# Kernel tuning notes

Hardware: AMD Instinct MI355X
Metric: run time of the kernel (lower is better)

## Reference

```python
import jax, jax.numpy as jnp
import numpy as np

EMBED_DIM = 1024
NUM_HEADS = 16
HEAD_DIM = EMBED_DIM // NUM_HEADS
EPSILON = 1e-6
SCORE_SCALE = 1.0
B, L = 2, 2048


def setup_inputs() -> dict:
    key = jax.random.key(0)
    k0, k1, k2, k3, k4 = jax.random.split(key, 5)
    s_in = 1.0 / np.sqrt(EMBED_DIM)
    return {
        "x": jax.random.normal(k0, (B, L, EMBED_DIM), dtype=jnp.float32),
        "w_qkv": jax.random.normal(k1, (EMBED_DIM, 3 * EMBED_DIM), dtype=jnp.float32) * s_in,
        "b_qkv": jnp.zeros((3 * EMBED_DIM,), dtype=jnp.float32),
        "w_out": jax.random.normal(k2, (EMBED_DIM, EMBED_DIM), dtype=jnp.float32) * s_in,
        "b_out": jnp.zeros((EMBED_DIM,), dtype=jnp.float32),
    }


def reference(x, w_qkv, b_qkv, w_out, b_out):
    Bq, Lq, E = x.shape
    qkv = x @ w_qkv + b_qkv  # [B, L, 3E]
    q, k, v = jnp.split(qkv, 3, axis=-1)
    q = q.reshape(Bq, Lq, NUM_HEADS, HEAD_DIM).transpose(0, 2, 1, 3)  # bhld
    k = k.reshape(Bq, Lq, NUM_HEADS, HEAD_DIM).transpose(0, 2, 1, 3)
    v = v.reshape(Bq, Lq, NUM_HEADS, HEAD_DIM).transpose(0, 2, 1, 3)

    dot = jnp.einsum('bhid,bhjd->bhij', q, k)
    q_norm_sq = jnp.sum(q * q, axis=-1, keepdims=True)          # [b,h,L,1]
    k_norm_sq = jnp.sum(k * k, axis=-1, keepdims=True)          # [b,h,L,1]
    vals = q_norm_sq + k_norm_sq.transpose(0, 1, 3, 2)          # [b,h,L,L]
    scores = (dot * dot) / (vals - 2.0 * dot + EPSILON) * SCORE_SCALE

    mask = jnp.triu(jnp.ones((Lq, Lq), dtype=scores.dtype), k=1) * -1e9
    scores = scores + mask[None, None, :, :]
    attn = jax.nn.softmax(scores, axis=-1)
    out = jnp.einsum('bhij,bhjd->bhid', attn, v)
    out = out.transpose(0, 2, 1, 3).reshape(Bq, Lq, E)
    return out @ w_out + b_out
```

## Files before the change

kernel.cpp:

```cpp
#include <hip/hip_runtime.h>

#define EMBED 1024
#define NH 16
#define HD 64
#define SEQ 2048
#define BATCH 2
#define ROWS (BATCH*SEQ)
#define BHD (BATCH*NH)

typedef __bf16 bf16x8 __attribute__((ext_vector_type(8)));
typedef _Float16 f16x4 __attribute__((ext_vector_type(4)));
typedef float f32x4 __attribute__((ext_vector_type(4)));

__device__ __forceinline__ unsigned short f2bf(float f){
  union { float f; unsigned u; } v; v.f = f;
  unsigned r = v.u + 0x7fffu + ((v.u >> 16) & 1u);
  return (unsigned short)(r >> 16);
}
__device__ __forceinline__ float bf2f(unsigned short s){
  union { unsigned u; float f; } v; v.u = ((unsigned)s) << 16; return v.f;
}
__device__ __forceinline__ unsigned short f2h(float f){
  union { _Float16 h; unsigned short u; } v; v.h = (_Float16)f; return v.u;
}

typedef __attribute__((address_space(1))) unsigned int as1_t;
typedef __attribute__((address_space(3))) unsigned int as3_t;
__device__ __forceinline__ void async_ld16(const void* gp, void* lp){
  __builtin_amdgcn_global_load_lds((as1_t*)gp, (as3_t*)lp, 16, 0, 0);
}


__global__ __launch_bounds__(256) void k_conv(const float* __restrict__ x,
                                              unsigned short* __restrict__ xb, int n4){
  int i = blockIdx.x * blockDim.x + threadIdx.x;
  if (i < n4){
    float4 f = ((const float4*)x)[i];
    ushort4 o;
    o.x = f2bf(f.x); o.y = f2bf(f.y); o.z = f2bf(f.z); o.w = f2bf(f.w);
    ((ushort4*)xb)[i] = o;
  }
}

__global__ __launch_bounds__(256) void k_tr_f2b(const float* __restrict__ in,
                                                unsigned short* __restrict__ out, int R, int C){
  __shared__ float t[32][33];
  int c0 = blockIdx.x * 32, r0 = blockIdx.y * 32;
  int tx = threadIdx.x, ty = threadIdx.y;
  #pragma unroll
  for (int i = 0; i < 4; i++){ int r = ty + i*8; t[r][tx] = in[(size_t)(r0+r)*C + c0 + tx]; }
  __syncthreads();
  #pragma unroll
  for (int i = 0; i < 4; i++){ int rr = ty + i*8; out[(size_t)(c0+rr)*R + r0 + tx] = f2bf(t[tx][rr]); }
}

__global__ __launch_bounds__(256) void k_tr_b2b(const unsigned short* __restrict__ in,
                                                unsigned short* __restrict__ out, int R, int C){
  in  += (size_t)blockIdx.z * R * C;
  out += (size_t)blockIdx.z * R * C;
  __shared__ unsigned short t[32][33];
  int c0 = blockIdx.x * 32, r0 = blockIdx.y * 32;
  int tx = threadIdx.x, ty = threadIdx.y;
  #pragma unroll
  for (int i = 0; i < 4; i++){ int r = ty + i*8; t[r][tx] = in[(size_t)(r0+r)*C + c0 + tx]; }
  __syncthreads();
  #pragma unroll
  for (int i = 0; i < 4; i++){ int rr = ty + i*8; out[(size_t)(c0+rr)*R + r0 + tx] = t[tx][rr]; }
}

__global__ __launch_bounds__(256) void k_norms(const unsigned short* __restrict__ q,
                                               const unsigned short* __restrict__ k,
                                               float* __restrict__ qn, float* __restrict__ kn){
  int i = blockIdx.x * blockDim.x + threadIdx.x;
  const uint4* qr = (const uint4*)(q + (size_t)i * HD);
  const uint4* kr = (const uint4*)(k + (size_t)i * HD);
  float sq = 0.f, sk = 0.f;
  #pragma unroll
  for (int t = 0; t < 8; t++){
    uint4 uq = qr[t], uk = kr[t];
    unsigned aq[4] = {uq.x, uq.y, uq.z, uq.w};
    unsigned ak[4] = {uk.x, uk.y, uk.z, uk.w};
    #pragma unroll
    for (int j = 0; j < 4; j++){
      float f0 = bf2f((unsigned short)(aq[j] & 0xffff));
      float f1 = bf2f((unsigned short)(aq[j] >> 16));
      sq += f0*f0 + f1*f1;
      float g0 = bf2f((unsigned short)(ak[j] & 0xffff));
      float g1 = bf2f((unsigned short)(ak[j] >> 16));
      sk += g0*g0 + g1*g1;
    }
  }
  qn[i] = sq; kn[i] = sk;
}


__global__ __launch_bounds__(256) void k_gemm_qkv(
    const unsigned short* __restrict__ A,
    const unsigned short* __restrict__ BT,
    const float* __restrict__ bias,
    unsigned short* __restrict__ qo, unsigned short* __restrict__ ko,
    unsigned short* __restrict__ vo)
{
  __shared__ __align__(16) unsigned short As[128*32];
  __shared__ __align__(16) unsigned short Bs[128*32];
  const int K = EMBED;
  int m0 = blockIdx.x * 128, n0 = blockIdx.y * 128;
  int tid = threadIdx.x, lane = tid & 63, wave = tid >> 6;
  int wm = wave >> 1, wn = wave & 1;
  int l16 = lane & 15, quad = lane >> 4;
  f32x4 acc[4][4] = {};
  int c0i = wave*64 + lane, c1i = 256 + wave*64 + lane;
  int r0 = c0i >> 2, cc0 = (c0i & 3) * 8;
  int r1 = c1i >> 2, cc1 = (c1i & 3) * 8;
  unsigned short* lA0 = &As[(wave*64)*8];
  unsigned short* lA1 = &As[(256 + wave*64)*8];
  unsigned short* lB0 = &Bs[(wave*64)*8];
  unsigned short* lB1 = &Bs[(256 + wave*64)*8];
  for (int k0 = 0; k0 < K; k0 += 32){
    async_ld16((void*)&A [(size_t)(m0 + r0)*K + k0 + cc0], (void*)lA0);
    async_ld16((void*)&A [(size_t)(m0 + r1)*K + k0 + cc1], (void*)lA1);
    async_ld16((void*)&BT[(size_t)(n0 + r0)*K + k0 + cc0], (void*)lB0);
    async_ld16((void*)&BT[(size_t)(n0 + r1)*K + k0 + cc1], (void*)lB1);
    __syncthreads();
    bf16x8 af[4], bfr[4];
    #pragma unroll
    for (int mi = 0; mi < 4; mi++) af[mi]  = *(const bf16x8*)&As[(wm*64 + mi*16 + l16)*32 + quad*8];
    #pragma unroll
    for (int ni = 0; ni < 4; ni++) bfr[ni] = *(const bf16x8*)&Bs[(wn*64 + ni*16 + l16)*32 + quad*8];
    #pragma unroll
    for (int mi = 0; mi < 4; mi++)
      #pragma unroll
      for (int ni = 0; ni < 4; ni++)
        acc[mi][ni] = __builtin_amdgcn_mfma_f32_16x16x32_bf16(af[mi], bfr[ni], acc[mi][ni], 0, 0, 0);
    __syncthreads();
  }
  #pragma unroll
  for (int mi = 0; mi < 4; mi++)
    #pragma unroll
    for (int ni = 0; ni < 4; ni++)
      #pragma unroll
      for (int rr = 0; rr < 4; rr++){
        int row = m0 + wm*64 + mi*16 + quad*4 + rr;
        int col = n0 + wn*64 + ni*16 + l16;
        float val = acc[mi][ni][rr] + bias[col];
        int b = row >> 11, l = row & 2047;
        int which = col >> 10, e = col & 1023, h = e >> 6, d = e & 63;
        unsigned short* dst = which == 0 ? qo : (which == 1 ? ko : vo);
        unsigned short bits = (which == 2) ? f2h(val) : f2bf(val);
        dst[(((size_t)(b*NH + h))*SEQ + l)*HD + d] = bits;
      }
}


__global__ __launch_bounds__(256) void k_attn(
    const unsigned short* __restrict__ qg,
    const unsigned short* __restrict__ kg,
    const unsigned short* __restrict__ vtg,
    const float* __restrict__ qn,
    const float* __restrict__ kn,
    unsigned short* __restrict__ attn_out)
{
  __shared__ __align__(16) unsigned short Ks[2][2048];
  __shared__ __align__(16) _Float16      Vs[2][2048];
  int bh = blockIdx.y; int b = bh >> 4, h = bh & 15;
  int tid = threadIdx.x, lane = tid & 63, wave = tid >> 6;
  int l16 = lane & 15, quad = lane >> 4;
  int tb = 31 - blockIdx.x;
  int qb = tb * 64;
  int q0 = qb + wave*16;
  int jmax_w = q0 + 16;
  int jmax_b = qb + 64;

  const unsigned short* qbase = qg  + (size_t)bh * SEQ * HD;
  const unsigned short* kbase = kg  + (size_t)bh * SEQ * HD;
  const _Float16*       vtb   = (const _Float16*)vtg + (size_t)bh * HD * SEQ;
  const float* knb = kn + (size_t)bh * SEQ;

  int sI = wave*64 + lane;
  int kj   = sI >> 3;
  int ko16 = (sI & 7) ^ (kj & 7);
  int vd   = sI >> 2;
  int vc2  = (sI & 3) ^ (vd & 3);

  bf16x8 aq[2];
  #pragma unroll
  for (int sk = 0; sk < 2; sk++)
    aq[sk] = *(const bf16x8*)&qbase[(size_t)(q0 + l16)*HD + sk*32 + quad*8];
  float qn_m = qn[(size_t)bh*SEQ + q0 + l16];

  float m_run = -1e30f, l_lane = 0.f;
  f32x4 oacc[4] = {};

  async_ld16((const void*)&kbase[(size_t)kj*HD + ko16*8], (void*)&Ks[0][wave*512]);
  async_ld16((const void*)&vtb[(size_t)vd*SEQ + vc2*8],   (void*)&Vs[0][wave*512]);

  for (int j0 = 0; j0 < jmax_b; j0 += 32){
    int buf = (j0 >> 5) & 1;
    __syncthreads();
    if (j0 + 32 < jmax_b){
      async_ld16((const void*)&kbase[(size_t)(j0 + 32 + kj)*HD + ko16*8], (void*)&Ks[buf^1][wave*512]);
      async_ld16((const void*)&vtb[(size_t)vd*SEQ + (j0 + 32) + vc2*8],   (void*)&Vs[buf^1][wave*512]);
    }
    if (j0 < jmax_w){
      f32x4 st[2] = {};
      #pragma unroll
      for (int tile = 0; tile < 2; tile++)
        #pragma unroll
        for (int sk = 0; sk < 2; sk++){
          bf16x8 ak = *(const bf16x8*)&Ks[buf][((tile*16 + l16)*8 + ((sk*4 + quad) ^ (l16 & 7)))*8];
          st[tile] = __builtin_amdgcn_mfma_f32_16x16x32_bf16(ak, aq[sk], st[tile], 0, 0, 0);
        }
      float4 kn_a = *(const float4*)&knb[j0 + quad*4];
      float4 kn_b = *(const float4*)&knb[j0 + 16 + quad*4];
      float kn_j[2][4] = {{kn_a.x, kn_a.y, kn_a.z, kn_a.w}, {kn_b.x, kn_b.y, kn_b.z, kn_b.w}};
      int mg = q0 + l16;
      float sc[2][4];
      if (j0 + 32 > q0){
        #pragma unroll
        for (int tile = 0; tile < 2; tile++)
          #pragma unroll
          for (int rr = 0; rr < 4; rr++){
            int jg = j0 + tile*16 + quad*4 + rr;
            float dot = st[tile][rr];
            float den = fmaxf(qn_m + kn_j[tile][rr] - 2.0f*dot, 0.0f) + 1e-6f;
            float v = dot * dot * __builtin_amdgcn_rcpf(den);
            sc[tile][rr] = (jg <= mg) ? v : -1e30f;
          }
      } else {
        #pragma unroll
        for (int tile = 0; tile < 2; tile++)
          #pragma unroll
          for (int rr = 0; rr < 4; rr++){
            float dot = st[tile][rr];
            float den = fmaxf(qn_m + kn_j[tile][rr] - 2.0f*dot, 0.0f) + 1e-6f;
            sc[tile][rr] = dot * dot * __builtin_amdgcn_rcpf(den);
          }
      }
      float mx = fmaxf(fmaxf(fmaxf(sc[0][0], sc[0][1]), fmaxf(sc[0][2], sc[0][3])),
                       fmaxf(fmaxf(sc[1][0], sc[1][1]), fmaxf(sc[1][2], sc[1][3])));
      mx = fmaxf(mx, __shfl_xor(mx, 16));
      mx = fmaxf(mx, __shfl_xor(mx, 32));
      float mnew = fmaxf(m_run, mx);
      float alpha = __expf(m_run - mnew);
      m_run = mnew;

      float ps = 0.f;
      #pragma unroll
      for (int tile = 0; tile < 2; tile++)
        #pragma unroll
        for (int rr = 0; rr < 4; rr++){
          float e = __expf(sc[tile][rr] - mnew);
          sc[tile][rr] = e; ps += e;
        }
      l_lane = l_lane * alpha + ps;

      #pragma unroll
      for (int g = 0; g < 4; g++)
        #pragma unroll
        for (int rr = 0; rr < 4; rr++) oacc[g][rr] *= alpha;

      #pragma unroll
      for (int tile = 0; tile < 2; tile++){
        f16x4 pf;
        #pragma unroll
        for (int rr = 0; rr < 4; rr++) pf[rr] = (_Float16)sc[tile][rr];
        #pragma unroll
        for (int g = 0; g < 4; g++){
          f16x4 av = *(const f16x4*)&Vs[buf][(g*16 + l16)*32 + (((tile*2 + (quad>>1)) ^ (l16 & 3))*8) + (quad & 1)*4];
          oacc[g] = __builtin_amdgcn_mfma_f32_16x16x16f16(av, pf, oacc[g], 0, 0, 0);
        }
      }
    }
  }

  float l_tot = l_lane + __shfl_xor(l_lane, 16);
  l_tot += __shfl_xor(l_tot, 32);
  float linv = __builtin_amdgcn_rcpf(l_tot);

  size_t orow = (size_t)(b*SEQ + q0 + l16)*EMBED + h*HD;
  #pragma unroll
  for (int g = 0; g < 4; g++){
    ushort4 pk;
    pk.x = f2bf(oacc[g][0] * linv);
    pk.y = f2bf(oacc[g][1] * linv);
    pk.z = f2bf(oacc[g][2] * linv);
    pk.w = f2bf(oacc[g][3] * linv);
    *(ushort4*)&attn_out[orow + g*16 + quad*4] = pk;
  }
}


__global__ __launch_bounds__(256) void k_gemm_out(
    const unsigned short* __restrict__ A,
    const unsigned short* __restrict__ BT,
    const float* __restrict__ bias,
    float* __restrict__ out)
{
  __shared__ __align__(16) unsigned short As[128*32];
  __shared__ __align__(16) unsigned short Bs[128*32];
  const int K = EMBED;
  int m0 = blockIdx.x * 128, n0 = blockIdx.y * 128;
  int tid = threadIdx.x, lane = tid & 63, wave = tid >> 6;
  int wm = wave >> 1, wn = wave & 1;
  int l16 = lane & 15, quad = lane >> 4;
  f32x4 acc[4][4] = {};
  int c0i = wave*64 + lane, c1i = 256 + wave*64 + lane;
  int r0 = c0i >> 2, cc0 = (c0i & 3) * 8;
  int r1 = c1i >> 2, cc1 = (c1i & 3) * 8;
  unsigned short* lA0 = &As[(wave*64)*8];
  unsigned short* lA1 = &As[(256 + wave*64)*8];
  unsigned short* lB0 = &Bs[(wave*64)*8];
  unsigned short* lB1 = &Bs[(256 + wave*64)*8];
  for (int k0 = 0; k0 < K; k0 += 32){
    async_ld16((void*)&A [(size_t)(m0 + r0)*K + k0 + cc0], (void*)lA0);
    async_ld16((void*)&A [(size_t)(m0 + r1)*K + k0 + cc1], (void*)lA1);
    async_ld16((void*)&BT[(size_t)(n0 + r0)*K + k0 + cc0], (void*)lB0);
    async_ld16((void*)&BT[(size_t)(n0 + r1)*K + k0 + cc1], (void*)lB1);
    __syncthreads();
    bf16x8 af[4], bfr[4];
    #pragma unroll
    for (int mi = 0; mi < 4; mi++) af[mi]  = *(const bf16x8*)&As[(wm*64 + mi*16 + l16)*32 + quad*8];
    #pragma unroll
    for (int ni = 0; ni < 4; ni++) bfr[ni] = *(const bf16x8*)&Bs[(wn*64 + ni*16 + l16)*32 + quad*8];
    #pragma unroll
    for (int mi = 0; mi < 4; mi++)
      #pragma unroll
      for (int ni = 0; ni < 4; ni++)
        acc[mi][ni] = __builtin_amdgcn_mfma_f32_16x16x32_bf16(af[mi], bfr[ni], acc[mi][ni], 0, 0, 0);
    __syncthreads();
  }
  #pragma unroll
  for (int mi = 0; mi < 4; mi++)
    #pragma unroll
    for (int ni = 0; ni < 4; ni++)
      #pragma unroll
      for (int rr = 0; rr < 4; rr++){
        int row = m0 + wm*64 + mi*16 + quad*4 + rr;
        int col = n0 + wn*64 + ni*16 + l16;
        out[(size_t)row*EMBED + col] = acc[mi][ni][rr] + bias[col];
      }
}


extern "C" void kernel_launch(void* const* d_in, const int* in_sizes, int n_in,
                              void* d_out, int out_size, void* d_ws, size_t ws_size,
                              hipStream_t stream) {
  const float* x     = (const float*)d_in[0];
  const float* w_qkv = (const float*)d_in[1];
  const float* b_qkv = (const float*)d_in[2];
  const float* w_out = (const float*)d_in[3];
  const float* b_out = (const float*)d_in[4];
  float* out = (float*)d_out;

  char* ws = (char*)d_ws;
  size_t off = 0;
  auto alloc = [&](size_t bytes) -> void* {
    void* p = ws + off; off += (bytes + 255) & ~(size_t)255; return p;
  };
  unsigned short* xb    = (unsigned short*)alloc((size_t)ROWS * EMBED * 2);
  unsigned short* wqkvT = (unsigned short*)alloc((size_t)3 * EMBED * EMBED * 2);
  unsigned short* woutT = (unsigned short*)alloc((size_t)EMBED * EMBED * 2);
  unsigned short* qb    = (unsigned short*)alloc((size_t)ROWS * EMBED * 2);
  unsigned short* kb    = (unsigned short*)alloc((size_t)ROWS * EMBED * 2);
  unsigned short* vb    = (unsigned short*)alloc((size_t)ROWS * EMBED * 2);
  unsigned short* vTb   = (unsigned short*)alloc((size_t)ROWS * EMBED * 2);
  float* qn = (float*)alloc((size_t)BHD * SEQ * 4);
  float* kn = (float*)alloc((size_t)BHD * SEQ * 4);
  unsigned short* attnb = xb;

  k_conv<<<dim3((ROWS*EMBED/4 + 255)/256), dim3(256), 0, stream>>>(x, xb, ROWS*EMBED/4);
  k_tr_f2b<<<dim3(3*EMBED/32, EMBED/32), dim3(32, 8), 0, stream>>>(w_qkv, wqkvT, EMBED, 3*EMBED);
  k_tr_f2b<<<dim3(EMBED/32, EMBED/32), dim3(32, 8), 0, stream>>>(w_out, woutT, EMBED, EMBED);
  k_gemm_qkv<<<dim3(ROWS/128, 3*EMBED/128), dim3(256), 0, stream>>>(xb, wqkvT, b_qkv, qb, kb, vb);
  k_norms<<<dim3(BHD*SEQ/256), dim3(256), 0, stream>>>(qb, kb, qn, kn);
  k_tr_b2b<<<dim3(HD/32, SEQ/32, BHD), dim3(32, 8), 0, stream>>>(vb, vTb, SEQ, HD);
  k_attn<<<dim3(32, BHD), dim3(256), 0, stream>>>(qb, kb, vTb, qn, kn, attnb);
  k_gemm_out<<<dim3(ROWS/128, EMBED/128), dim3(256), 0, stream>>>(attnb, woutT, b_out, out);
}
```

Measured before the change: 271.2 us.

## Pair causal query tiles per block and stage K/V through registers

The attention kernel now runs 128-thread blocks. Each block processes two 32-row query tiles, t=p and t=63-p, one after the other, so the causal work per block is balanced. The async direct-to-LDS loads with XOR swizzle are replaced by register-staged global loads written to padded shared arrays (row strides 72 and 36), with the next tile's loads issued before compute. This aims to remove the triangular load imbalance and the swizzle overhead. In exchange it halves the threads per block and adds register pressure plus an extra sync per pass.

```diff
diff --git a/kernel.cpp b/kernel.cpp
--- a/kernel.cpp
+++ b/kernel.cpp
@@ -152,7 +152,7 @@
 }
 
 
-__global__ __launch_bounds__(256) void k_attn(
+__global__ __launch_bounds__(128) void k_attn(
     const unsigned short* __restrict__ qg,
     const unsigned short* __restrict__ kg,
     const unsigned short* __restrict__ vtg,
@@ -160,132 +160,156 @@
     const float* __restrict__ kn,
     unsigned short* __restrict__ attn_out)
 {
-  __shared__ __align__(16) unsigned short Ks[2][2048];
-  __shared__ __align__(16) _Float16      Vs[2][2048];
+  __shared__ __align__(16) unsigned short Ks[2][32*72];
+  __shared__ __align__(16) _Float16      Vs[2][64*36];
   int bh = blockIdx.y; int b = bh >> 4, h = bh & 15;
   int tid = threadIdx.x, lane = tid & 63, wave = tid >> 6;
   int l16 = lane & 15, quad = lane >> 4;
-  int tb = 31 - blockIdx.x;
-  int qb = tb * 64;
-  int q0 = qb + wave*16;
-  int jmax_w = q0 + 16;
-  int jmax_b = qb + 64;
+  int p = blockIdx.x;
 
   const unsigned short* qbase = qg  + (size_t)bh * SEQ * HD;
   const unsigned short* kbase = kg  + (size_t)bh * SEQ * HD;
   const _Float16*       vtb   = (const _Float16*)vtg + (size_t)bh * HD * SEQ;
   const float* knb = kn + (size_t)bh * SEQ;
 
-  int sI = wave*64 + lane;
-  int kj   = sI >> 3;
-  int ko16 = (sI & 7) ^ (kj & 7);
-  int vd   = sI >> 2;
-  int vc2  = (sI & 3) ^ (vd & 3);
-
-  bf16x8 aq[2];
-  #pragma unroll
-  for (int sk = 0; sk < 2; sk++)
-    aq[sk] = *(const bf16x8*)&qbase[(size_t)(q0 + l16)*HD + sk*32 + quad*8];
-  float qn_m = qn[(size_t)bh*SEQ + q0 + l16];
-
-  float m_run = -1e30f, l_lane = 0.f;
-  f32x4 oacc[4] = {};
-
-  async_ld16((const void*)&kbase[(size_t)kj*HD + ko16*8], (void*)&Ks[0][wave*512]);
-  async_ld16((const void*)&vtb[(size_t)vd*SEQ + vc2*8],   (void*)&Vs[0][wave*512]);
-
-  for (int j0 = 0; j0 < jmax_b; j0 += 32){
-    int buf = (j0 >> 5) & 1;
-    __syncthreads();
-    if (j0 + 32 < jmax_b){
-      async_ld16((const void*)&kbase[(size_t)(j0 + 32 + kj)*HD + ko16*8], (void*)&Ks[buf^1][wave*512]);
-      async_ld16((const void*)&vtb[(size_t)vd*SEQ + (j0 + 32) + vc2*8],   (void*)&Vs[buf^1][wave*512]);
+  int kd0 = tid >> 3,        kc0 = tid & 7;
+  int kd1 = (tid + 128) >> 3, kc1 = tid & 7;
+  int vd0 = tid >> 2,        vc0 = tid & 3;
+  int vd1 = 32 + (tid >> 2), vc1 = tid & 3;
+
+  #pragma unroll
+  for (int pass = 0; pass < 2; pass++){
+    int t = pass ? (63 - p) : p;
+    int q0 = t*32 + wave*16;
+    int jmax_w = q0 + 16;
+    int jmax_b = t*32 + 32;
+
+    bf16x8 aq[2];
+    #pragma unroll
+    for (int sk = 0; sk < 2; sk++)
+      aq[sk] = *(const bf16x8*)&qbase[(size_t)(q0 + l16)*HD + sk*32 + quad*8];
+    float qn_m = qn[(size_t)bh*SEQ + q0 + l16];
+
+    float m_run = -1e30f, l_lane = 0.f;
+    f32x4 oacc[4] = {};
+
+    {
+      uint4 ka = *(const uint4*)&kbase[(size_t)kd0*HD + kc0*8];
+      uint4 kb = *(const uint4*)&kbase[(size_t)kd1*HD + kc1*8];
+      uint4 va = *(const uint4*)&vtb[(size_t)vd0*SEQ + vc0*8];
+      uint4 vb = *(const uint4*)&vtb[(size_t)vd1*SEQ + vc1*8];
+      *(uint4*)&Ks[0][kd0*72 + kc0*8] = ka;
+      *(uint4*)&Ks[0][kd1*72 + kc1*8] = kb;
+      *(uint2*)&Vs[0][vd0*36 + vc0*8]     = make_uint2(va.x, va.y);
+      *(uint2*)&Vs[0][vd0*36 + vc0*8 + 4] = make_uint2(va.z, va.w);
+      *(uint2*)&Vs[0][vd1*36 + vc1*8]     = make_uint2(vb.x, vb.y);
+      *(uint2*)&Vs[0][vd1*36 + vc1*8 + 4] = make_uint2(vb.z, vb.w);
     }
-    if (j0 < jmax_w){
-      f32x4 st[2] = {};
-      #pragma unroll
-      for (int tile = 0; tile < 2; tile++)
-        #pragma unroll
-        for (int sk = 0; sk < 2; sk++){
-          bf16x8 ak = *(const bf16x8*)&Ks[buf][((tile*16 + l16)*8 + ((sk*4 + quad) ^ (l16 & 7)))*8];
-          st[tile] = __builtin_amdgcn_mfma_f32_16x16x32_bf16(ak, aq[sk], st[tile], 0, 0, 0);
-        }
-      float4 kn_a = *(const float4*)&knb[j0 + quad*4];
-      float4 kn_b = *(const float4*)&knb[j0 + 16 + quad*4];
-      float kn_j[2][4] = {{kn_a.x, kn_a.y, kn_a.z, kn_a.w}, {kn_b.x, kn_b.y, kn_b.z, kn_b.w}};
-      int mg = q0 + l16;
-      float sc[2][4];
-      if (j0 + 32 > q0){
+    __syncthreads();
+
+    for (int j0 = 0; j0 < jmax_b; j0 += 32){
+      int buf = (j0 >> 5) & 1;
+      int jn = (j0 + 32 < jmax_b) ? j0 + 32 : j0;
+      uint4 ka = *(const uint4*)&kbase[(size_t)(jn + kd0)*HD + kc0*8];
+      uint4 kb = *(const uint4*)&kbase[(size_t)(jn + kd1)*HD + kc1*8];
+      uint4 va = *(const uint4*)&vtb[(size_t)vd0*SEQ + jn + vc0*8];
+      uint4 vb = *(const uint4*)&vtb[(size_t)vd1*SEQ + jn + vc1*8];
+
+      if (j0 < jmax_w){
+        f32x4 st[2] = {};
         #pragma unroll
         for (int tile = 0; tile < 2; tile++)
           #pragma unroll
-          for (int rr = 0; rr < 4; rr++){
-            int jg = j0 + tile*16 + quad*4 + rr;
-            float dot = st[tile][rr];
-            float den = fmaxf(qn_m + kn_j[tile][rr] - 2.0f*dot, 0.0f) + 1e-6f;
-            float v = dot * dot * __builtin_amdgcn_rcpf(den);
-            sc[tile][rr] = (jg <= mg) ? v : -1e30f;
+          for (int sk = 0; sk < 2; sk++){
+            bf16x8 ak = *(const bf16x8*)&Ks[buf][(tile*16 + l16)*72 + (sk*4 + quad)*8];
+            st[tile] = __builtin_amdgcn_mfma_f32_16x16x32_bf16(ak, aq[sk], st[tile], 0, 0, 0);
           }
-      } else {
+        float4 kn_a = *(const float4*)&knb[j0 + quad*4];
+        float4 kn_b = *(const float4*)&knb[j0 + 16 + quad*4];
+        float kn_j[2][4] = {{kn_a.x, kn_a.y, kn_a.z, kn_a.w}, {kn_b.x, kn_b.y, kn_b.z, kn_b.w}};
+        int mg = q0 + l16;
+        float sc[2][4];
+        if (j0 + 32 > q0){
+          #pragma unroll
+          for (int tile = 0; tile < 2; tile++)
+            #pragma unroll
+            for (int rr = 0; rr < 4; rr++){
+              int jg = j0 + tile*16 + quad*4 + rr;
+              float dot = st[tile][rr];
+              float den = fmaxf(qn_m + kn_j[tile][rr] - 2.0f*dot, 0.0f) + 1e-6f;
+              float v = dot * dot * __builtin_amdgcn_rcpf(den);
+              sc[tile][rr] = (jg <= mg) ? v : -1e30f;
+            }
+        } else {
+          #pragma unroll
+          for (int tile = 0; tile < 2; tile++)
+            #pragma unroll
+            for (int rr = 0; rr < 4; rr++){
+              float dot = st[tile][rr];
+              float den = fmaxf(qn_m + kn_j[tile][rr] - 2.0f*dot, 0.0f) + 1e-6f;
+              sc[tile][rr] = dot * dot * __builtin_amdgcn_rcpf(den);
+            }
+        }
+        float mx = fmaxf(fmaxf(fmaxf(sc[0][0], sc[0][1]), fmaxf(sc[0][2], sc[0][3])),
+                         fmaxf(fmaxf(sc[1][0], sc[1][1]), fmaxf(sc[1][2], sc[1][3])));
+        mx = fmaxf(mx, __shfl_xor(mx, 16));
+        mx = fmaxf(mx, __shfl_xor(mx, 32));
+        float mnew = fmaxf(m_run, mx);
+        float alpha = __expf(m_run - mnew);
+        m_run = mnew;
+
+        float ps = 0.f;
         #pragma unroll
         for (int tile = 0; tile < 2; tile++)
           #pragma unroll
           for (int rr = 0; rr < 4; rr++){
-            float dot = st[tile][rr];
-            float den = fmaxf(qn_m + kn_j[tile][rr] - 2.0f*dot, 0.0f) + 1e-6f;
-            sc[tile][rr] = dot * dot * __builtin_amdgcn_rcpf(den);
+            float e = __expf(sc[tile][rr] - mnew);
+            sc[tile][rr] = e; ps += e;
           }
-      }
-      float mx = fmaxf(fmaxf(fmaxf(sc[0][0], sc[0][1]), fmaxf(sc[0][2], sc[0][3])),
-                       fmaxf(fmaxf(sc[1][0], sc[1][1]), fmaxf(sc[1][2], sc[1][3])));
-      mx = fmaxf(mx, __shfl_xor(mx, 16));
-      mx = fmaxf(mx, __shfl_xor(mx, 32));
-      float mnew = fmaxf(m_run, mx);
-      float alpha = __expf(m_run - mnew);
-      m_run = mnew;
-
-      float ps = 0.f;
-      #pragma unroll
-      for (int tile = 0; tile < 2; tile++)
+        l_lane = l_lane * alpha + ps;
+
         #pragma unroll
-        for (int rr = 0; rr < 4; rr++){
-          float e = __expf(sc[tile][rr] - mnew);
-          sc[tile][rr] = e; ps += e;
-        }
-      l_lane = l_lane * alpha + ps;
-
-      #pragma unroll
-      for (int g = 0; g < 4; g++)
+        for (int g = 0; g < 4; g++)
+          #pragma unroll
+          for (int rr = 0; rr < 4; rr++) oacc[g][rr] *= alpha;
+
         #pragma unroll
-        for (int rr = 0; rr < 4; rr++) oacc[g][rr] *= alpha;
-
-      #pragma unroll
-      for (int tile = 0; tile < 2; tile++){
-        f16x4 pf;
-        #pragma unroll
-        for (int rr = 0; rr < 4; rr++) pf[rr] = (_Float16)sc[tile][rr];
-        #pragma unroll
-        for (int g = 0; g < 4; g++){
-          f16x4 av = *(const f16x4*)&Vs[buf][(g*16 + l16)*32 + (((tile*2 + (quad>>1)) ^ (l16 & 3))*8) + (quad & 1)*4];
-          oacc[g] = __builtin_amdgcn_mfma_f32_16x16x16f16(av, pf, oacc[g], 0, 0, 0);
+        for (int tile = 0; tile < 2; tile++){
+          f16x4 pf;
+          #pragma unroll
+          for (int rr = 0; rr < 4; rr++) pf[rr] = (_Float16)sc[tile][rr];
+          #pragma unroll
+          for (int g = 0; g < 4; g++){
+            f16x4 av = *(const f16x4*)&Vs[buf][(g*16 + l16)*36 + (tile*4 + quad)*4];
+            oacc[g] = __builtin_amdgcn_mfma_f32_16x16x16f16(av, pf, oacc[g], 0, 0, 0);
+          }
         }
       }
+
+      *(uint4*)&Ks[buf^1][kd0*72 + kc0*8] = ka;
+      *(uint4*)&Ks[buf^1][kd1*72 + kc1*8] = kb;
+      *(uint2*)&Vs[buf^1][vd0*36 + vc0*8]     = make_uint2(va.x, va.y);
+      *(uint2*)&Vs[buf^1][vd0*36 + vc0*8 + 4] = make_uint2(va.z, va.w);
+      *(uint2*)&Vs[buf^1][vd1*36 + vc1*8]     = make_uint2(vb.x, vb.y);
+      *(uint2*)&Vs[buf^1][vd1*36 + vc1*8 + 4] = make_uint2(vb.z, vb.w);
+      __syncthreads();
     }
-  }
-
-  float l_tot = l_lane + __shfl_xor(l_lane, 16);
-  l_tot += __shfl_xor(l_tot, 32);
-  float linv = __builtin_amdgcn_rcpf(l_tot);
-
-  size_t orow = (size_t)(b*SEQ + q0 + l16)*EMBED + h*HD;
-  #pragma unroll
-  for (int g = 0; g < 4; g++){
-    ushort4 pk;
-    pk.x = f2bf(oacc[g][0] * linv);
-    pk.y = f2bf(oacc[g][1] * linv);
-    pk.z = f2bf(oacc[g][2] * linv);
-    pk.w = f2bf(oacc[g][3] * linv);
-    *(ushort4*)&attn_out[orow + g*16 + quad*4] = pk;
+
+    float l_tot = l_lane + __shfl_xor(l_lane, 16);
+    l_tot += __shfl_xor(l_tot, 32);
+    float linv = __builtin_amdgcn_rcpf(l_tot);
+
+    size_t orow = (size_t)(b*SEQ + q0 + l16)*EMBED + h*HD;
+    #pragma unroll
+    for (int g = 0; g < 4; g++){
+      ushort4 pk;
+      pk.x = f2bf(oacc[g][0] * linv);
+      pk.y = f2bf(oacc[g][1] * linv);
+      pk.z = f2bf(oacc[g][2] * linv);
+      pk.w = f2bf(oacc[g][3] * linv);
+      *(ushort4*)&attn_out[orow + g*16 + quad*4] = pk;
+    }
+    __syncthreads();
   }
 }
 
@@ -374,6 +398,6 @@
   k_gemm_qkv<<<dim3(ROWS/128, 3*EMBED/128), dim3(256), 0, stream>>>(xb, wqkvT, b_qkv, qb, kb, vb);
   k_norms<<<dim3(BHD*SEQ/256), dim3(256), 0, stream>>>(qb, kb, qn, kn);
   k_tr_b2b<<<dim3(HD/32, SEQ/32, BHD), dim3(32, 8), 0, stream>>>(vb, vTb, SEQ, HD);
-  k_attn<<<dim3(32, BHD), dim3(256), 0, stream>>>(qb, kb, vTb, qn, kn, attnb);
+  k_attn<<<dim3(32, BHD), dim3(128), 0, stream>>>(qb, kb, vTb, qn, kn, attnb);
   k_gemm_out<<<dim3(ROWS/128, EMBED/128), dim3(256), 0, stream>>>(attnb, woutT, b_out, out);
 }
```

Result: faster. 246.6 us (-9.1%).
